# Performance work log

Measured on AMD Instinct MI355X. Metric: run time of the kernel, lower is better.

The kernel has to match this reference:

```python
import jax, jax.numpy as jnp
import numpy as np

B, N, C = 2, 8192, 256
H = 8
CH = C // H  # head dim 32
M = 32       # nbhd size
HID = 512    # mlp hidden = 2.0 * dim
TAB = 3025   # pre_table rows (55x55 relative positions)
POSF = 5     # pos_dim + 3


def _ln(x, w, b):
    mu = jnp.mean(x, axis=-1, keepdims=True)
    var = jnp.var(x, axis=-1, keepdims=True)
    return (x - mu) / jnp.sqrt(var + 1e-5) * w + b


def setup_inputs() -> dict:
    key = jax.random.key(0)
    ks = jax.random.split(key, 24)
    s = lambda fan: 1.0 / np.sqrt(fan)
    inp = {
        'feat': jax.random.normal(ks[0], (B, N, C), jnp.float32),
        'member_idx': jax.random.randint(ks[1], (B, N, M), 0, N),
        'cluster_mask': jnp.ones((B, N, M), jnp.float32),
        'pe_idx': jax.random.randint(ks[2], (B, N, M), 0, TAB),
        'global_attn': 0,
        'pre_table': jax.random.normal(ks[3], (TAB, POSF), jnp.float32),
        'norm1_w': jnp.ones((C,), jnp.float32),
        'norm1_b': jnp.zeros((C,), jnp.float32),
        'q_w': jax.random.normal(ks[4], (C, C), jnp.float32) * s(C),
        'q_b': jnp.zeros((C,), jnp.float32),
        'kv_w': jax.random.normal(ks[5], (2 * C, C), jnp.float32) * s(C),
        'kv_b': jnp.zeros((2 * C,), jnp.float32),
        'blank_k': jax.random.normal(ks[6], (C,), jnp.float32),
        'blank_v': jax.random.normal(ks[7], (C,), jnp.float32),
        'pe_w': jax.random.normal(ks[8], (H, POSF), jnp.float32) * s(POSF),
        'pe_b': jnp.zeros((H,), jnp.float32),
        'proj_w': jax.random.normal(ks[9], (C, C), jnp.float32) * s(C),
        'proj_b': jnp.zeros((C,), jnp.float32),
        'norm2_w': jnp.ones((C,), jnp.float32),
        'norm2_b': jnp.zeros((C,), jnp.float32),
        'fc1_w': jax.random.normal(ks[10], (HID, C), jnp.float32) * s(C),
        'fc1_b': jnp.zeros((HID,), jnp.float32),
        'fc2_w': jax.random.normal(ks[11], (C, HID), jnp.float32) * s(HID),
        'fc2_b': jnp.zeros((C,), jnp.float32),
    }
    return inp


def _block(feat, member_idx, cluster_mask, pe_idx, pre_table,
           norm1_w, norm1_b, q_w, q_b, kv_w, kv_b, blank_k, blank_v,
           pe_w, pe_b, proj_w, proj_b, norm2_w, norm2_b,
           fc1_w, fc1_b, fc2_w, fc2_b):
    b, n, c = feat.shape
    h, c_ = H, c // H
    scale = c_ ** -0.5
    shortcut = feat
    x = _ln(feat, norm1_w, norm1_b)
    q = (x @ q_w.T + q_b) * scale                     # b n c
    kv = (x @ kv_w.T + kv_b).reshape(b, n, h, 2, c_)  # torch view layout
    k = kv[..., 0, :]                                 # b n h c_
    v = kv[..., 1, :]
    q = q.reshape(b, n, h, c_)
    bidx = jnp.arange(b)[:, None, None]
    k_g = k[bidx, member_idx]                         # b n m h c_ (gather)
    attn = jnp.einsum('bnhc,bnmhc->bhnm', q, k_g)     # CLUSTENQK
    pe_table = pre_table @ pe_w.T + pe_b              # TAB h
    pos = pe_table[pe_idx]                            # b n m h
    attn = attn + pos.transpose(0, 3, 1, 2)
    attn = attn + (1.0 - cluster_mask)[:, None, :, :] * (-100.0)
    blank = jnp.einsum('bnhc,hc->bhn', q, blank_k.reshape(h, c_))
    blank = jnp.clip(blank, -5.0, 5.0)[..., None]     # b h n 1
    attn = jnp.concatenate([attn, blank], axis=-1)
    attn = jax.nn.softmax(attn, axis=-1)
    blank_a = attn[..., -1:]
    attn = attn[..., :-1]
    v_g = v[bidx, member_idx]                         # b n m h c_
    out = jnp.einsum('bhnm,bnmhc->bnhc', attn, v_g)   # CLUSTENAV
    out = out + blank_a.transpose(0, 2, 1, 3) * blank_v.reshape(1, 1, h, c_)
    out = out.reshape(b, n, c)
    out = out @ proj_w.T + proj_b
    x = shortcut + out
    y = _ln(x, norm2_w, norm2_b)
    y = jax.nn.gelu(y @ fc1_w.T + fc1_b, approximate=False)
    y = y @ fc2_w.T + fc2_b
    return x + y


def reference(feat, member_idx, cluster_mask, pe_idx, global_attn, pre_table,
              norm1_w, norm1_b, q_w, q_b, kv_w, kv_b, blank_k, blank_v,
              pe_w, pe_b, proj_w, proj_b, norm2_w, norm2_b,
              fc1_w, fc1_b, fc2_w, fc2_b):
    # global_attn is False (local cluster attention path)
    return _block(feat, member_idx, cluster_mask, pe_idx, pre_table,
                  norm1_w, norm1_b, q_w, q_b, kv_w, kv_b, blank_k, blank_v,
                  pe_w, pe_b, proj_w, proj_b, norm2_w, norm2_b,
                  fc1_w, fc1_b, fc2_w, fc2_b)
```

## Files before the change

### kernel.cpp

```cpp
#include <hip/hip_runtime.h>
#include <math.h>

namespace {
constexpr int kN    = 8192;
constexpr int kC    = 256;
constexpr int kRowsTotal = 2 * kN;
constexpr float kScale = 0.17677669529663687f;
}

typedef __attribute__((ext_vector_type(8))) short bf16x8;
typedef __attribute__((ext_vector_type(4))) float f32x4;
typedef _Float16 h8 __attribute__((ext_vector_type(8)));
typedef _Float16 h4 __attribute__((ext_vector_type(4)));

__device__ __forceinline__ unsigned short f2bf(float f) {
  unsigned int u = __float_as_uint(f);
  u += 0x7fffu + ((u >> 16) & 1u);
  return (unsigned short)(u >> 16);
}
__device__ __forceinline__ float bflo(unsigned int u) {
  return __uint_as_float(u << 16);
}
__device__ __forceinline__ float bfhi(unsigned int u) {
  return __uint_as_float(u & 0xffff0000u);
}
__device__ __forceinline__ unsigned short f2h(float f) {
  _Float16 h = (_Float16)f;
  unsigned short u;
  __builtin_memcpy(&u, &h, 2);
  return u;
}
__device__ __forceinline__ float h2f(unsigned short u) {
  _Float16 h;
  __builtin_memcpy(&h, &u, 2);
  return (float)h;
}

#define GLOAD16(g, l)                                                   \
  __builtin_amdgcn_global_load_lds(                                     \
      (const __attribute__((address_space(1))) void*)(g),               \
      (__attribute__((address_space(3))) void*)(l), 16, 0, 0)

__global__ __launch_bounds__(256) void prep_kernel(
    const float* __restrict__ qw, const float* __restrict__ kvw,
    const float* __restrict__ pjw, const float* __restrict__ f1w,
    const float* __restrict__ f2w, const float* __restrict__ qb,
    const float* __restrict__ kvb, const float* __restrict__ bk,
    const float* __restrict__ feat, const float* __restrict__ n1w,
    const float* __restrict__ n1b, const int* __restrict__ pe_idx,
    const float* __restrict__ pre_table, const float* __restrict__ pe_w,
    const float* __restrict__ pe_b, const float* __restrict__ cmask,
    unsigned short* __restrict__ wqkv, unsigned short* __restrict__ wproj,
    unsigned short* __restrict__ wfc1, unsigned short* __restrict__ wfc2,
    float* __restrict__ bqkv, unsigned short* __restrict__ bkh,
    unsigned short* __restrict__ xln, unsigned short* __restrict__ posm) {
  int bid = blockIdx.x;
  int t = threadIdx.x;
  if (bid < 2052) {
    int i = bid * 256 + t;
    if (i < 65536)       wqkv[i]            = f2bf(qw[i]);
    else if (i < 196608) wqkv[i]            = f2bf(kvw[i - 65536]);
    else if (i < 262144) wproj[i - 196608]  = f2bf(pjw[i - 196608]);
    else if (i < 393216) wfc1[i - 262144]   = f2bf(f1w[i - 262144]);
    else if (i < 524288) wfc2[i - 393216]   = f2bf(f2w[i - 393216]);
    else if (i < 524544) bqkv[i - 524288]   = qb[i - 524288];
    else if (i < 525056) bqkv[i - 524288]   = kvb[i - 524544];
    else if (i < 525312) bkh[i - 525056]    = f2h(bk[i - 525056]);
  } else if (bid < 6148) {
    int row = (bid - 2052) * 4 + (t >> 6);
    int l = t & 63;
    float4 v = *(const float4*)(feat + (size_t)row * kC + l * 4);
    float s  = v.x + v.y + v.z + v.w;
    float s2 = v.x * v.x + v.y * v.y + v.z * v.z + v.w * v.w;
#pragma unroll
    for (int d = 1; d < 64; d <<= 1) {
      s  += __shfl_xor(s, d, 64);
      s2 += __shfl_xor(s2, d, 64);
    }
    float mu = s * (1.0f / kC);
    float rstd = rsqrtf(s2 * (1.0f / kC) - mu * mu + 1e-5f);
    float4 wv = *(const float4*)(n1w + l * 4);
    float4 bv = *(const float4*)(n1b + l * 4);
    uint2 ov;
    ov.x = ((unsigned int)f2bf((v.y - mu) * rstd * wv.y + bv.y) << 16) |
           f2bf((v.x - mu) * rstd * wv.x + bv.x);
    ov.y = ((unsigned int)f2bf((v.w - mu) * rstd * wv.w + bv.w) << 16) |
           f2bf((v.z - mu) * rstd * wv.z + bv.z);
    *(uint2*)(xln + (size_t)row * kC + l * 4) = ov;
  } else {
    int i = (bid - 6148) * 256 + t;
    int row = i >> 8, m = (i >> 3) & 31, h = i & 7;
    int idx = pe_idx[(size_t)row * 32 + m];
    float acc = pe_b[h];
#pragma unroll
    for (int f = 0; f < 5; ++f)
      acc += pre_table[idx * 5 + f] * pe_w[h * 5 + f];
    acc += (1.0f - cmask[(size_t)row * 32 + m]) * -100.0f;
    posm[(size_t)row * 256 + h * 32 + m] = f2h(acc);
  }
}

template <int EPI, int KDIM>
__global__ __launch_bounds__(512) void gemm64(
    const unsigned short* __restrict__ A, const unsigned short* __restrict__ Wt,
    const float* __restrict__ bias, void* __restrict__ o1,
    unsigned short* __restrict__ o2, unsigned short* __restrict__ o3) {
  __shared__ alignas(16) unsigned short smem[40960];
  unsigned short* As0 = smem;
  unsigned short* Bs0 = smem + 8192;
  int t = threadIdx.x;
  int w = t >> 6, l = t & 63;
  int bm = blockIdx.x * 64, bn = blockIdx.y * 256;

  f32x4 acc[4][2] = {};

  const size_t aoff = (size_t)(bm + w * 8 + (l >> 3)) * KDIM + (l & 7) * 8;
  const size_t boff = (size_t)(bn + w * 32 + (l >> 3)) * KDIM + (l & 7) * 8;
  const int lr = l & 15, lk = l >> 4;

#define STAGE_T(buf, k0)                                                      \
  do {                                                                        \
    GLOAD16(A + aoff + (k0), As0 + (buf)*4096 + w * 512 + l * 8);             \
    GLOAD16(Wt + boff + (k0), Bs0 + (buf)*16384 + w * 2048 + l * 8);          \
    GLOAD16(Wt + boff + (k0) + (size_t)8 * KDIM,                              \
            Bs0 + (buf)*16384 + w * 2048 + 512 + l * 8);                      \
    GLOAD16(Wt + boff + (k0) + (size_t)16 * KDIM,                             \
            Bs0 + (buf)*16384 + w * 2048 + 1024 + l * 8);                     \
    GLOAD16(Wt + boff + (k0) + (size_t)24 * KDIM,                             \
            Bs0 + (buf)*16384 + w * 2048 + 1536 + l * 8);                     \
  } while (0)

  auto compute = [&](int buf) {
#pragma unroll
    for (int kk = 0; kk < 2; ++kk) {
      bf16x8 af[4], bfr[2];
#pragma unroll
      for (int mi = 0; mi < 4; ++mi)
        af[mi] = *(const bf16x8*)(As0 + buf * 4096 + (mi * 16 + lr) * 64 +
                                  kk * 32 + lk * 8);
#pragma unroll
      for (int ni = 0; ni < 2; ++ni)
        bfr[ni] = *(const bf16x8*)(Bs0 + buf * 16384 +
                                   (w * 32 + ni * 16 + lr) * 64 + kk * 32 +
                                   lk * 8);
#pragma unroll
      for (int mi = 0; mi < 4; ++mi)
#pragma unroll
        for (int ni = 0; ni < 2; ++ni)
          acc[mi][ni] = __builtin_amdgcn_mfma_f32_16x16x32_bf16(
              af[mi], bfr[ni], acc[mi][ni], 0, 0, 0);
    }
  };

  STAGE_T(0, 0);
  __syncthreads();
  int cur = 0;
#pragma unroll
  for (int k0 = 64; k0 < KDIM; k0 += 64) {
    STAGE_T(cur ^ 1, k0);
    compute(cur);
    __syncthreads();
    cur ^= 1;
  }
  compute(cur);

#pragma unroll
  for (int mi = 0; mi < 4; ++mi) {
#pragma unroll
    for (int ni = 0; ni < 2; ++ni) {
      int col = bn + w * 32 + ni * 16 + lr;
      float bv = bias[col];
#pragma unroll
      for (int j = 0; j < 4; ++j) {
        int rg = bm + mi * 16 + lk * 4 + j;
        float x = acc[mi][ni][j] + bv;
        if (col < 256) {
          ((unsigned short*)o1)[(size_t)rg * 256 + col] = f2h(x * kScale);
        } else {
          int c = col - 256;
          int h = c >> 6, sbit = (c >> 5) & 1, ch = c & 31;
          unsigned short* dst = sbit ? o3 : o2;
          dst[(size_t)rg * 256 + h * 32 + ch] = f2h(x);
        }
      }
    }
  }
#undef STAGE_T
}

__global__ __launch_bounds__(512) void mlp_fused(
    const unsigned short* __restrict__ A,
    const unsigned short* __restrict__ Wp,
    const float* __restrict__ pbias,
    const float* __restrict__ feat,
    const float* __restrict__ w2, const float* __restrict__ b2,
    const unsigned short* __restrict__ W1, const float* __restrict__ b1,
    const unsigned short* __restrict__ W2, const float* __restrict__ b2f,
    float* __restrict__ outp) {
  __shared__ alignas(16) unsigned short sm[66560];
  int t = threadIdx.x;
  int w = t >> 6, l = t & 63;
  int bm = blockIdx.x * 64;
  const int lr = l & 15, lk = l >> 4;

  f32x4 accp[4][2] = {};
  {
    const size_t aoff = (size_t)(bm + w * 8 + (l >> 3)) * 256 + (l & 7) * 8;
    const size_t boff = (size_t)(w * 32 + (l >> 3)) * 256 + (l & 7) * 8;
#define PSTAGE(buf, k0)                                                       \
  do {                                                                        \
    GLOAD16(A + aoff + (k0), sm + (buf)*4096 + w * 512 + l * 8);              \
    GLOAD16(Wp + boff + (k0), sm + 8192 + (buf)*16384 + w * 2048 + l * 8);    \
    GLOAD16(Wp + boff + (k0) + (size_t)2048,                                  \
            sm + 8192 + (buf)*16384 + w * 2048 + 512 + l * 8);                \
    GLOAD16(Wp + boff + (k0) + (size_t)4096,                                  \
            sm + 8192 + (buf)*16384 + w * 2048 + 1024 + l * 8);               \
    GLOAD16(Wp + boff + (k0) + (size_t)6144,                                  \
            sm + 8192 + (buf)*16384 + w * 2048 + 1536 + l * 8);               \
  } while (0)
    auto computeP = [&](int buf) {
#pragma unroll
      for (int kk = 0; kk < 2; ++kk) {
        bf16x8 af[4], bfr[2];
#pragma unroll
        for (int mi = 0; mi < 4; ++mi)
          af[mi] = *(const bf16x8*)(sm + buf * 4096 + (mi * 16 + lr) * 64 +
                                    kk * 32 + lk * 8);
#pragma unroll
        for (int ni = 0; ni < 2; ++ni)
          bfr[ni] = *(const bf16x8*)(sm + 8192 + buf * 16384 +
                                     (w * 32 + ni * 16 + lr) * 64 + kk * 32 +
                                     lk * 8);
#pragma unroll
        for (int mi = 0; mi < 4; ++mi)
#pragma unroll
          for (int ni = 0; ni < 2; ++ni)
            accp[mi][ni] = __builtin_amdgcn_mfma_f32_16x16x32_bf16(
                af[mi], bfr[ni], accp[mi][ni], 0, 0, 0);
      }
    };
    PSTAGE(0, 0);
    __syncthreads();
    int cur = 0;
#pragma unroll
    for (int k0 = 64; k0 < 256; k0 += 64) {
      PSTAGE(cur ^ 1, k0);
      computeP(cur);
      __syncthreads();
      cur ^= 1;
    }
    computeP(cur);
#undef PSTAGE
  }

  f32x4 xr[4][2];
  float* xs = (float*)sm;
  __syncthreads();
#pragma unroll
  for (int mi = 0; mi < 4; ++mi) {
#pragma unroll
    for (int ni = 0; ni < 2; ++ni) {
      int c = w * 32 + ni * 16 + lr;
      float bv = pbias[c];
#pragma unroll
      for (int j = 0; j < 4; ++j) {
        int rl = mi * 16 + lk * 4 + j;
        float x = accp[mi][ni][j] + bv + feat[(size_t)(bm + rl) * 256 + c];
        xr[mi][ni][j] = x;
        xs[rl * 260 + c] = x;
      }
    }
  }
  __syncthreads();

  {
    int r = t >> 3, sub = t & 7;
    float4 xv[8];
    float sx = 0.f, sxx = 0.f;
#pragma unroll
    for (int i = 0; i < 8; ++i) {
      xv[i] = *(const float4*)&xs[r * 260 + sub * 4 + i * 32];
      sx  += xv[i].x + xv[i].y + xv[i].z + xv[i].w;
      sxx += xv[i].x * xv[i].x + xv[i].y * xv[i].y + xv[i].z * xv[i].z +
             xv[i].w * xv[i].w;
    }
#pragma unroll
    for (int d = 1; d < 8; d <<= 1) {
      sx  += __shfl_xor(sx, d, 64);
      sxx += __shfl_xor(sxx, d, 64);
    }
    float mu = sx * (1.0f / 256.0f);
    float rstd = rsqrtf(sxx * (1.0f / 256.0f) - mu * mu + 1e-5f);
#pragma unroll
    for (int i = 0; i < 8; ++i) {
      int c = sub * 4 + i * 32;
      float4 wv = *(const float4*)(w2 + c);
      float4 bv = *(const float4*)(b2 + c);
      uint2 ov;
      ov.x = ((unsigned int)f2bf((xv[i].y - mu) * rstd * wv.y + bv.y) << 16) |
             f2bf((xv[i].x - mu) * rstd * wv.x + bv.x);
      ov.y = ((unsigned int)f2bf((xv[i].w - mu) * rstd * wv.w + bv.w) << 16) |
             f2bf((xv[i].z - mu) * rstd * wv.z + bv.z);
      *(uint2*)&sm[49664 + r * 264 + c] = ov;
    }
  }
  __syncthreads();

  const int FB = 33280;
#define F1STAGE(buf, k0, c)                                                   \
  do {                                                                        \
    GLOAD16(W1 + (size_t)((c)*256 + w * 32 + (l >> 2)) * 256 + (k0) +         \
                (l & 3) * 8,                                                  \
            sm + FB + (buf)*8192 + w * 1024 + l * 8);                         \
    GLOAD16(W1 + (size_t)((c)*256 + w * 32 + 16 + (l >> 2)) * 256 + (k0) +    \
                (l & 3) * 8,                                                  \
            sm + FB + (buf)*8192 + w * 1024 + 512 + l * 8);                   \
  } while (0)
#pragma unroll
  for (int c = 0; c < 2; ++c) {
    f32x4 accf[4][2] = {};
    auto computeF1 = [&](int buf, int ka) {
      bf16x8 af[4], bfr[2];
#pragma unroll
      for (int mi = 0; mi < 4; ++mi)
        af[mi] =
            *(const bf16x8*)(sm + 49664 + (mi * 16 + lr) * 264 + ka + lk * 8);
#pragma unroll
      for (int ni = 0; ni < 2; ++ni)
        bfr[ni] = *(const bf16x8*)(sm + FB + buf * 8192 +
                                   (w * 32 + ni * 16 + lr) * 32 + lk * 8);
#pragma unroll
      for (int mi = 0; mi < 4; ++mi)
#pragma unroll
        for (int ni = 0; ni < 2; ++ni)
          accf[mi][ni] = __builtin_amdgcn_mfma_f32_16x16x32_bf16(
              af[mi], bfr[ni], accf[mi][ni], 0, 0, 0);
    };
    F1STAGE(0, 0, c);
    __syncthreads();
    int cur = 0;
#pragma unroll
    for (int k0 = 32; k0 < 256; k0 += 32) {
      F1STAGE(cur ^ 1, k0, c);
      computeF1(cur, k0 - 32);
      __syncthreads();
      cur ^= 1;
    }
    computeF1(cur, 224);
    __syncthreads();
#pragma unroll
    for (int mi = 0; mi < 4; ++mi) {
#pragma unroll
      for (int ni = 0; ni < 2; ++ni) {
        int colg = c * 256 + w * 32 + ni * 16 + lr;
        float bv = b1[colg];
#pragma unroll
        for (int j = 0; j < 4; ++j) {
          float x = accf[mi][ni][j] + bv;
          float g = 0.5f * x * (1.0f + erff(x * 0.70710678118654752f));
          sm[(mi * 16 + lk * 4 + j) * 520 + colg] = f2bf(g);
        }
      }
    }
  }
#undef F1STAGE
  __syncthreads();

  f32x4 acc2[4][2] = {};
#define F2STAGE(buf, k0)                                                      \
  do {                                                                        \
    GLOAD16(W2 + (size_t)(w * 32 + (l >> 3)) * 512 + (k0) + (l & 7) * 8,      \
            sm + FB + (buf)*16384 + w * 2048 + l * 8);                        \
    GLOAD16(W2 + (size_t)(w * 32 + 8 + (l >> 3)) * 512 + (k0) + (l & 7) * 8,  \
            sm + FB + (buf)*16384 + w * 2048 + 512 + l * 8);                  \
    GLOAD16(W2 + (size_t)(w * 32 + 16 + (l >> 3)) * 512 + (k0) + (l & 7) * 8, \
            sm + FB + (buf)*16384 + w * 2048 + 1024 + l * 8);                 \
    GLOAD16(W2 + (size_t)(w * 32 + 24 + (l >> 3)) * 512 + (k0) + (l & 7) * 8, \
            sm + FB + (buf)*16384 + w * 2048 + 1536 + l * 8);                 \
  } while (0)
  {
    auto computeF2 = [&](int buf, int ka) {
#pragma unroll
      for (int kk = 0; kk < 2; ++kk) {
        bf16x8 af[4], bfr[2];
#pragma unroll
        for (int mi = 0; mi < 4; ++mi)
          af[mi] = *(const bf16x8*)(sm + (mi * 16 + lr) * 520 + ka + kk * 32 +
                                    lk * 8);
#pragma unroll
        for (int ni = 0; ni < 2; ++ni)
          bfr[ni] = *(const bf16x8*)(sm + FB + buf * 16384 +
                                     (w * 32 + ni * 16 + lr) * 64 + kk * 32 +
                                     lk * 8);
#pragma unroll
        for (int mi = 0; mi < 4; ++mi)
#pragma unroll
          for (int ni = 0; ni < 2; ++ni)
            acc2[mi][ni] = __builtin_amdgcn_mfma_f32_16x16x32_bf16(
                af[mi], bfr[ni], acc2[mi][ni], 0, 0, 0);
      }
    };
    F2STAGE(0, 0);
    __syncthreads();
    int cur = 0;
#pragma unroll
    for (int k0 = 64; k0 < 512; k0 += 64) {
      F2STAGE(cur ^ 1, k0);
      computeF2(cur, k0 - 64);
      __syncthreads();
      cur ^= 1;
    }
    computeF2(cur, 448);
  }
#undef F2STAGE

#pragma unroll
  for (int mi = 0; mi < 4; ++mi) {
#pragma unroll
    for (int ni = 0; ni < 2; ++ni) {
      int col = w * 32 + ni * 16 + lr;
      float bv = b2f[col];
#pragma unroll
      for (int j = 0; j < 4; ++j) {
        int rg = bm + mi * 16 + lk * 4 + j;
        outp[(size_t)rg * 256 + col] = xr[mi][ni][j] + acc2[mi][ni][j] + bv;
      }
    }
  }
}

__global__ __launch_bounds__(256) void attn_kernel(
    const unsigned short* __restrict__ q, const unsigned short* __restrict__ k,
    const unsigned short* __restrict__ v, const int* __restrict__ member_idx,
    const unsigned short* __restrict__ posm,
    const unsigned short* __restrict__ bkh, const float* __restrict__ blank_v,
    unsigned short* __restrict__ outp) {
  int t = threadIdx.x;
  int w = t >> 6, l = t & 63;
  int bid = blockIdx.x;
  int part = bid & 7;
  int bb = part >> 2, hg = part & 3;
  int row = bb * kN + (bid >> 3) * 4 + w;
  const unsigned int kvbyte = (unsigned int)bb * (kN * 512u);

  __shared__ float        aw[4][2][36];
  __shared__ unsigned int offs[4][32];
  __shared__ float        posl[4][2][32];

  {
    int m = l & 31, hloc = l >> 5;
    posl[w][hloc][m] = h2f(posm[(size_t)row * 256 + hg * 64 + l]);
    if (l < 32)
      offs[w][l] =
          kvbyte + (unsigned int)member_idx[(size_t)row * 32 + l] * 512u;
  }
  __syncthreads();

  const int m8 = l >> 3, ch = l & 7;
  const int hsel = ch >> 2;

  h8 qv8 = *(const h8*)(q + (size_t)row * 256 + hg * 64 + ch * 8);

  float lg[4];
#pragma unroll
  for (int i = 0; i < 4; ++i) {
    int mi = i * 8 + m8;
    const char* kp = (const char*)k + offs[w][mi] + hg * 128 + ch * 16;
    h8 kv = *(const h8*)kp;
    float p = 0.f;
#pragma unroll
    for (int e = 0; e < 8; ++e) p = fmaf((float)qv8[e], (float)kv[e], p);
    p += __shfl_xor(p, 1, 64);
    p += __shfl_xor(p, 2, 64);
    lg[i] = p + posl[w][hsel][mi];
  }

  float bl = 0.f;
  {
    h8 bk8 = *(const h8*)(bkh + hg * 64 + ch * 8);
#pragma unroll
    for (int e = 0; e < 8; ++e) bl = fmaf((float)qv8[e], (float)bk8[e], bl);
    bl += __shfl_xor(bl, 1, 64);
    bl += __shfl_xor(bl, 2, 64);
    bl = fminf(fmaxf(bl, -5.0f), 5.0f);
  }

  float mx = fmaxf(fmaxf(lg[0], lg[1]), fmaxf(lg[2], lg[3]));
  mx = fmaxf(mx, __shfl_xor(mx, 8, 64));
  mx = fmaxf(mx, __shfl_xor(mx, 16, 64));
  mx = fmaxf(mx, __shfl_xor(mx, 32, 64));
  mx = fmaxf(mx, bl);
  float e4[4], s = 0.f;
#pragma unroll
  for (int i = 0; i < 4; ++i) { e4[i] = __expf(lg[i] - mx); s += e4[i]; }
  s += __shfl_xor(s, 8, 64);
  s += __shfl_xor(s, 16, 64);
  s += __shfl_xor(s, 32, 64);
  float eb = __expf(bl - mx);
  s += eb;
  float inv = __builtin_amdgcn_rcpf(s);
  if ((ch & 3) == 0) {
#pragma unroll
    for (int i = 0; i < 4; ++i) aw[w][hsel][i * 8 + m8] = e4[i] * inv;
    if (m8 == 0) aw[w][hsel][32] = eb * inv;
  }
  __syncthreads();

  const int hp = l >> 5, sq = (l >> 3) & 3, c8 = l & 7;
  const char* vb = (const char*)v + (hg * 2 + hp) * 64 + c8 * 8;
  float a0 = 0.f, a1 = 0.f, a2 = 0.f, a3 = 0.f;
#pragma unroll
  for (int i = 0; i < 8; ++i) {
    int mm = sq * 8 + i;
    float a = aw[w][hp][mm];
    h4 u = *(const h4*)(vb + offs[w][mm]);
    a0 = fmaf(a, (float)u[0], a0);
    a1 = fmaf(a, (float)u[1], a1);
    a2 = fmaf(a, (float)u[2], a2);
    a3 = fmaf(a, (float)u[3], a3);
  }
  a0 += __shfl_xor(a0, 8, 64);  a1 += __shfl_xor(a1, 8, 64);
  a2 += __shfl_xor(a2, 8, 64);  a3 += __shfl_xor(a3, 8, 64);
  a0 += __shfl_xor(a0, 16, 64); a1 += __shfl_xor(a1, 16, 64);
  a2 += __shfl_xor(a2, 16, 64); a3 += __shfl_xor(a3, 16, 64);
  if (sq == 0) {
    float ab = aw[w][hp][32];
    int c = (hg * 2 + hp) * 32 + c8 * 4;
    float4 bv = *(const float4*)(blank_v + c);
    a0 = fmaf(ab, bv.x, a0);
    a1 = fmaf(ab, bv.y, a1);
    a2 = fmaf(ab, bv.z, a2);
    a3 = fmaf(ab, bv.w, a3);
    uint2 o;
    o.x = ((unsigned int)f2bf(a1) << 16) | f2bf(a0);
    o.y = ((unsigned int)f2bf(a3) << 16) | f2bf(a2);
    *(uint2*)(outp + (size_t)row * 256 + c) = o;
  }
}

extern "C" void kernel_launch(void* const* d_in, const int* in_sizes, int n_in,
                              void* d_out, int out_size, void* d_ws, size_t ws_size,
                              hipStream_t stream) {
  const float* feat       = (const float*)d_in[0];
  const int*   member_idx = (const int*)d_in[1];
  const float* cmask      = (const float*)d_in[2];
  const int*   pe_idx     = (const int*)d_in[3];
  const float* pre_table  = (const float*)d_in[5];
  const float* n1w        = (const float*)d_in[6];
  const float* n1b        = (const float*)d_in[7];
  const float* q_w        = (const float*)d_in[8];
  const float* q_b        = (const float*)d_in[9];
  const float* kv_w       = (const float*)d_in[10];
  const float* kv_b       = (const float*)d_in[11];
  const float* blank_k    = (const float*)d_in[12];
  const float* blank_v    = (const float*)d_in[13];
  const float* pe_w       = (const float*)d_in[14];
  const float* pe_b       = (const float*)d_in[15];
  const float* proj_w     = (const float*)d_in[16];
  const float* proj_b     = (const float*)d_in[17];
  const float* n2w        = (const float*)d_in[18];
  const float* n2b        = (const float*)d_in[19];
  const float* fc1_w      = (const float*)d_in[20];
  const float* fc1_b      = (const float*)d_in[21];
  const float* fc2_w      = (const float*)d_in[22];
  const float* fc2_b      = (const float*)d_in[23];

  float* out = (float*)d_out;
  unsigned char* ws = (unsigned char*)d_ws;

  unsigned short* xln   = (unsigned short*)(ws + 0);
  unsigned short* q_buf = (unsigned short*)(ws + 8388608);
  unsigned short* k_buf = (unsigned short*)(ws + 16777216);
  unsigned short* v_buf = (unsigned short*)(ws + 25165824);
  unsigned short* wqkv  = (unsigned short*)(ws + 33554432);
  unsigned short* wproj = (unsigned short*)(ws + 33947648);
  unsigned short* wfc1  = (unsigned short*)(ws + 34078720);
  unsigned short* wfc2  = (unsigned short*)(ws + 34340864);
  float*          bqkv  = (float*)(ws + 34603008);
  unsigned short* bkh   = (unsigned short*)(ws + 34606080);
  unsigned short* attn_out = xln;
  unsigned short* posm  = (unsigned short*)out;

  prep_kernel<<<22532, 256, 0, stream>>>(
      q_w, kv_w, proj_w, fc1_w, fc2_w, q_b, kv_b, blank_k, feat, n1w, n1b,
      pe_idx, pre_table, pe_w, pe_b, cmask, wqkv, wproj, wfc1, wfc2, bqkv,
      bkh, xln, posm);

  gemm64<0, 256><<<dim3(kRowsTotal / 64, 3), 512, 0, stream>>>(
      xln, wqkv, bqkv, q_buf, k_buf, v_buf);

  attn_kernel<<<kRowsTotal, 256, 0, stream>>>(
      q_buf, k_buf, v_buf, member_idx, posm, bkh, blank_v, attn_out);

  mlp_fused<<<kRowsTotal / 64, 512, 0, stream>>>(
      attn_out, wproj, proj_b, feat, n2w, n2b, wfc1, fc1_b, wfc2, fc2_b, out);
}
```

Baseline: 108.7 us.

## Fuse LayerNorm1 into QKV GEMM and use fdot2 in attention logits

Removes the LayerNorm section from the prep kernel and computes LN1 inside a new qkv_fused kernel, which keeps the normalized 64-row A tile resident in shared memory and loops over the three output column blocks, streaming only weight tiles. This drops the bf16 xln round trip through global memory and one grid dimension, but each block now does three times the GEMM work serially, leaving fewer blocks (256) for the GPU. The attention kernel also replaces scalar f16-to-f32 FMAs with packed fdot2 instructions for the q·k and q·blank_k dot products.

```diff
diff --git a/kernel.cpp b/kernel.cpp
--- a/kernel.cpp
+++ b/kernel.cpp
@@ -12,17 +12,12 @@
 typedef __attribute__((ext_vector_type(4))) float f32x4;
 typedef _Float16 h8 __attribute__((ext_vector_type(8)));
 typedef _Float16 h4 __attribute__((ext_vector_type(4)));
+typedef _Float16 h2 __attribute__((ext_vector_type(2)));
 
 __device__ __forceinline__ unsigned short f2bf(float f) {
   unsigned int u = __float_as_uint(f);
   u += 0x7fffu + ((u >> 16) & 1u);
   return (unsigned short)(u >> 16);
-}
-__device__ __forceinline__ float bflo(unsigned int u) {
-  return __uint_as_float(u << 16);
-}
-__device__ __forceinline__ float bfhi(unsigned int u) {
-  return __uint_as_float(u & 0xffff0000u);
 }
 __device__ __forceinline__ unsigned short f2h(float f) {
   _Float16 h = (_Float16)f;
@@ -36,6 +31,16 @@
   return (float)h;
 }
 
+#if __has_builtin(__builtin_amdgcn_fdot2)
+__device__ __forceinline__ float fdot2f(h2 a, h2 b, float c) {
+  return __builtin_amdgcn_fdot2(a, b, c, false);
+}
+#else
+__device__ __forceinline__ float fdot2f(h2 a, h2 b, float c) {
+  return fmaf((float)a[0], (float)b[0], fmaf((float)a[1], (float)b[1], c));
+}
+#endif
+
 #define GLOAD16(g, l)                                                   \
   __builtin_amdgcn_global_load_lds(                                     \
       (const __attribute__((address_space(1))) void*)(g),               \
@@ -46,14 +51,12 @@
     const float* __restrict__ pjw, const float* __restrict__ f1w,
     const float* __restrict__ f2w, const float* __restrict__ qb,
     const float* __restrict__ kvb, const float* __restrict__ bk,
-    const float* __restrict__ feat, const float* __restrict__ n1w,
-    const float* __restrict__ n1b, const int* __restrict__ pe_idx,
-    const float* __restrict__ pre_table, const float* __restrict__ pe_w,
-    const float* __restrict__ pe_b, const float* __restrict__ cmask,
-    unsigned short* __restrict__ wqkv, unsigned short* __restrict__ wproj,
-    unsigned short* __restrict__ wfc1, unsigned short* __restrict__ wfc2,
-    float* __restrict__ bqkv, unsigned short* __restrict__ bkh,
-    unsigned short* __restrict__ xln, unsigned short* __restrict__ posm) {
+    const int* __restrict__ pe_idx, const float* __restrict__ pre_table,
+    const float* __restrict__ pe_w, const float* __restrict__ pe_b,
+    const float* __restrict__ cmask, unsigned short* __restrict__ wqkv,
+    unsigned short* __restrict__ wproj, unsigned short* __restrict__ wfc1,
+    unsigned short* __restrict__ wfc2, float* __restrict__ bqkv,
+    unsigned short* __restrict__ bkh, unsigned short* __restrict__ posm) {
   int bid = blockIdx.x;
   int t = threadIdx.x;
   if (bid < 2052) {
@@ -66,29 +69,8 @@
     else if (i < 524544) bqkv[i - 524288]   = qb[i - 524288];
     else if (i < 525056) bqkv[i - 524288]   = kvb[i - 524544];
     else if (i < 525312) bkh[i - 525056]    = f2h(bk[i - 525056]);
-  } else if (bid < 6148) {
-    int row = (bid - 2052) * 4 + (t >> 6);
-    int l = t & 63;
-    float4 v = *(const float4*)(feat + (size_t)row * kC + l * 4);
-    float s  = v.x + v.y + v.z + v.w;
-    float s2 = v.x * v.x + v.y * v.y + v.z * v.z + v.w * v.w;
-#pragma unroll
-    for (int d = 1; d < 64; d <<= 1) {
-      s  += __shfl_xor(s, d, 64);
-      s2 += __shfl_xor(s2, d, 64);
-    }
-    float mu = s * (1.0f / kC);
-    float rstd = rsqrtf(s2 * (1.0f / kC) - mu * mu + 1e-5f);
-    float4 wv = *(const float4*)(n1w + l * 4);
-    float4 bv = *(const float4*)(n1b + l * 4);
-    uint2 ov;
-    ov.x = ((unsigned int)f2bf((v.y - mu) * rstd * wv.y + bv.y) << 16) |
-           f2bf((v.x - mu) * rstd * wv.x + bv.x);
-    ov.y = ((unsigned int)f2bf((v.w - mu) * rstd * wv.w + bv.w) << 16) |
-           f2bf((v.z - mu) * rstd * wv.z + bv.z);
-    *(uint2*)(xln + (size_t)row * kC + l * 4) = ov;
   } else {
-    int i = (bid - 6148) * 256 + t;
+    int i = (bid - 2052) * 256 + t;
     int row = i >> 8, m = (i >> 3) & 31, h = i & 7;
     int idx = pe_idx[(size_t)row * 32 + m];
     float acc = pe_b[h];
@@ -100,99 +82,120 @@
   }
 }
 
-template <int EPI, int KDIM>
-__global__ __launch_bounds__(512) void gemm64(
-    const unsigned short* __restrict__ A, const unsigned short* __restrict__ Wt,
-    const float* __restrict__ bias, void* __restrict__ o1,
-    unsigned short* __restrict__ o2, unsigned short* __restrict__ o3) {
-  __shared__ alignas(16) unsigned short smem[40960];
-  unsigned short* As0 = smem;
-  unsigned short* Bs0 = smem + 8192;
+__global__ __launch_bounds__(512) void qkv_fused(
+    const float* __restrict__ feat, const float* __restrict__ n1w,
+    const float* __restrict__ n1b, const unsigned short* __restrict__ Wq,
+    const float* __restrict__ bqkv, unsigned short* __restrict__ qo,
+    unsigned short* __restrict__ ko, unsigned short* __restrict__ vo) {
+  __shared__ alignas(16) unsigned short sm[33280];
   int t = threadIdx.x;
   int w = t >> 6, l = t & 63;
-  int bm = blockIdx.x * 64, bn = blockIdx.y * 256;
-
-  f32x4 acc[4][2] = {};
-
-  const size_t aoff = (size_t)(bm + w * 8 + (l >> 3)) * KDIM + (l & 7) * 8;
-  const size_t boff = (size_t)(bn + w * 32 + (l >> 3)) * KDIM + (l & 7) * 8;
+  int bm = blockIdx.x * 64;
   const int lr = l & 15, lk = l >> 4;
-
-#define STAGE_T(buf, k0)                                                      \
+  const int BsB = 16896;
+
+  {
+    int r = t >> 3, sub = t & 7;
+    float4 xv[8];
+    float sx = 0.f, sxx = 0.f;
+#pragma unroll
+    for (int i = 0; i < 8; ++i) {
+      xv[i] = *(const float4*)(feat + (size_t)(bm + r) * 256 + sub * 4 + i * 32);
+      sx  += xv[i].x + xv[i].y + xv[i].z + xv[i].w;
+      sxx += xv[i].x * xv[i].x + xv[i].y * xv[i].y + xv[i].z * xv[i].z +
+             xv[i].w * xv[i].w;
+    }
+#pragma unroll
+    for (int d = 1; d < 8; d <<= 1) {
+      sx  += __shfl_xor(sx, d, 64);
+      sxx += __shfl_xor(sxx, d, 64);
+    }
+    float mu = sx * (1.0f / 256.0f);
+    float rstd = rsqrtf(sxx * (1.0f / 256.0f) - mu * mu + 1e-5f);
+#pragma unroll
+    for (int i = 0; i < 8; ++i) {
+      int c = sub * 4 + i * 32;
+      float4 wv = *(const float4*)(n1w + c);
+      float4 bv = *(const float4*)(n1b + c);
+      uint2 ov;
+      ov.x = ((unsigned int)f2bf((xv[i].y - mu) * rstd * wv.y + bv.y) << 16) |
+             f2bf((xv[i].x - mu) * rstd * wv.x + bv.x);
+      ov.y = ((unsigned int)f2bf((xv[i].w - mu) * rstd * wv.w + bv.w) << 16) |
+             f2bf((xv[i].z - mu) * rstd * wv.z + bv.z);
+      *(uint2*)&sm[r * 264 + c] = ov;
+    }
+  }
+
+#define QSTAGE(buf, k0, bn)                                                   \
   do {                                                                        \
-    GLOAD16(A + aoff + (k0), As0 + (buf)*4096 + w * 512 + l * 8);             \
-    GLOAD16(Wt + boff + (k0), Bs0 + (buf)*16384 + w * 2048 + l * 8);          \
-    GLOAD16(Wt + boff + (k0) + (size_t)8 * KDIM,                              \
-            Bs0 + (buf)*16384 + w * 2048 + 512 + l * 8);                      \
-    GLOAD16(Wt + boff + (k0) + (size_t)16 * KDIM,                             \
-            Bs0 + (buf)*16384 + w * 2048 + 1024 + l * 8);                     \
-    GLOAD16(Wt + boff + (k0) + (size_t)24 * KDIM,                             \
-            Bs0 + (buf)*16384 + w * 2048 + 1536 + l * 8);                     \
+    GLOAD16(Wq + (size_t)((bn)*256 + w * 32 + (l >> 2)) * 256 + (k0) +        \
+                (l & 3) * 8,                                                  \
+            sm + BsB + (buf)*8192 + w * 1024 + l * 8);                        \
+    GLOAD16(Wq + (size_t)((bn)*256 + w * 32 + 16 + (l >> 2)) * 256 + (k0) +   \
+                (l & 3) * 8,                                                  \
+            sm + BsB + (buf)*8192 + w * 1024 + 512 + l * 8);                  \
   } while (0)
 
-  auto compute = [&](int buf) {
-#pragma unroll
-    for (int kk = 0; kk < 2; ++kk) {
+#pragma unroll
+  for (int bn = 0; bn < 3; ++bn) {
+    f32x4 acc[4][2] = {};
+    auto computeQ = [&](int buf, int ka) {
       bf16x8 af[4], bfr[2];
 #pragma unroll
       for (int mi = 0; mi < 4; ++mi)
-        af[mi] = *(const bf16x8*)(As0 + buf * 4096 + (mi * 16 + lr) * 64 +
-                                  kk * 32 + lk * 8);
+        af[mi] = *(const bf16x8*)(sm + (mi * 16 + lr) * 264 + ka + lk * 8);
 #pragma unroll
       for (int ni = 0; ni < 2; ++ni)
-        bfr[ni] = *(const bf16x8*)(Bs0 + buf * 16384 +
-                                   (w * 32 + ni * 16 + lr) * 64 + kk * 32 +
-                                   lk * 8);
+        bfr[ni] = *(const bf16x8*)(sm + BsB + buf * 8192 + w * 1024 +
+                                   (ni * 16 + lr) * 32 + lk * 8);
 #pragma unroll
       for (int mi = 0; mi < 4; ++mi)
 #pragma unroll
         for (int ni = 0; ni < 2; ++ni)
           acc[mi][ni] = __builtin_amdgcn_mfma_f32_16x16x32_bf16(
               af[mi], bfr[ni], acc[mi][ni], 0, 0, 0);
-    }
-  };
-
-  STAGE_T(0, 0);
-  __syncthreads();
-  int cur = 0;
-#pragma unroll
-  for (int k0 = 64; k0 < KDIM; k0 += 64) {
-    STAGE_T(cur ^ 1, k0);
-    compute(cur);
+    };
+    QSTAGE(0, 0, bn);
     __syncthreads();
-    cur ^= 1;
-  }
-  compute(cur);
-
-#pragma unroll
-  for (int mi = 0; mi < 4; ++mi) {
-#pragma unroll
-    for (int ni = 0; ni < 2; ++ni) {
-      int col = bn + w * 32 + ni * 16 + lr;
-      float bv = bias[col];
-#pragma unroll
-      for (int j = 0; j < 4; ++j) {
-        int rg = bm + mi * 16 + lk * 4 + j;
-        float x = acc[mi][ni][j] + bv;
-        if (col < 256) {
-          ((unsigned short*)o1)[(size_t)rg * 256 + col] = f2h(x * kScale);
-        } else {
-          int c = col - 256;
-          int h = c >> 6, sbit = (c >> 5) & 1, ch = c & 31;
-          unsigned short* dst = sbit ? o3 : o2;
-          dst[(size_t)rg * 256 + h * 32 + ch] = f2h(x);
+    int cur = 0;
+#pragma unroll
+    for (int k0 = 32; k0 < 256; k0 += 32) {
+      QSTAGE(cur ^ 1, k0, bn);
+      computeQ(cur, k0 - 32);
+      __syncthreads();
+      cur ^= 1;
+    }
+    computeQ(cur, 224);
+
+#pragma unroll
+    for (int mi = 0; mi < 4; ++mi) {
+#pragma unroll
+      for (int ni = 0; ni < 2; ++ni) {
+        int col = bn * 256 + w * 32 + ni * 16 + lr;
+        float bv = bqkv[col];
+#pragma unroll
+        for (int j = 0; j < 4; ++j) {
+          int rg = bm + mi * 16 + lk * 4 + j;
+          float x = acc[mi][ni][j] + bv;
+          if (col < 256) {
+            qo[(size_t)rg * 256 + col] = f2h(x * kScale);
+          } else {
+            int c = col - 256;
+            int h = c >> 6, sbit = (c >> 5) & 1, ch = c & 31;
+            unsigned short* dst = sbit ? vo : ko;
+            dst[(size_t)rg * 256 + h * 32 + ch] = f2h(x);
+          }
         }
       }
     }
-  }
-#undef STAGE_T
+    __syncthreads();
+  }
+#undef QSTAGE
 }
 
 __global__ __launch_bounds__(512) void mlp_fused(
-    const unsigned short* __restrict__ A,
-    const unsigned short* __restrict__ Wp,
-    const float* __restrict__ pbias,
-    const float* __restrict__ feat,
+    const unsigned short* __restrict__ A, const unsigned short* __restrict__ Wp,
+    const float* __restrict__ pbias, const float* __restrict__ feat,
     const float* __restrict__ w2, const float* __restrict__ b2,
     const unsigned short* __restrict__ W1, const float* __restrict__ b1,
     const unsigned short* __restrict__ W2, const float* __restrict__ b2f,
@@ -460,6 +463,7 @@
   const int hsel = ch >> 2;
 
   h8 qv8 = *(const h8*)(q + (size_t)row * 256 + hg * 64 + ch * 8);
+  const h2* qa = (const h2*)&qv8;
 
   float lg[4];
 #pragma unroll
@@ -467,9 +471,10 @@
     int mi = i * 8 + m8;
     const char* kp = (const char*)k + offs[w][mi] + hg * 128 + ch * 16;
     h8 kv = *(const h8*)kp;
+    const h2* ka = (const h2*)&kv;
     float p = 0.f;
 #pragma unroll
-    for (int e = 0; e < 8; ++e) p = fmaf((float)qv8[e], (float)kv[e], p);
+    for (int e = 0; e < 4; ++e) p = fdot2f(qa[e], ka[e], p);
     p += __shfl_xor(p, 1, 64);
     p += __shfl_xor(p, 2, 64);
     lg[i] = p + posl[w][hsel][mi];
@@ -478,8 +483,9 @@
   float bl = 0.f;
   {
     h8 bk8 = *(const h8*)(bkh + hg * 64 + ch * 8);
-#pragma unroll
-    for (int e = 0; e < 8; ++e) bl = fmaf((float)qv8[e], (float)bk8[e], bl);
+    const h2* ba = (const h2*)&bk8;
+#pragma unroll
+    for (int e = 0; e < 4; ++e) bl = fdot2f(qa[e], ba[e], bl);
     bl += __shfl_xor(bl, 1, 64);
     bl += __shfl_xor(bl, 2, 64);
     bl = fminf(fmaxf(bl, -5.0f), 5.0f);
@@ -568,7 +574,7 @@
   float* out = (float*)d_out;
   unsigned char* ws = (unsigned char*)d_ws;
 
-  unsigned short* xln   = (unsigned short*)(ws + 0);
+  unsigned short* attn_out = (unsigned short*)(ws + 0);
   unsigned short* q_buf = (unsigned short*)(ws + 8388608);
   unsigned short* k_buf = (unsigned short*)(ws + 16777216);
   unsigned short* v_buf = (unsigned short*)(ws + 25165824);
@@ -578,16 +584,14 @@
   unsigned short* wfc2  = (unsigned short*)(ws + 34340864);
   float*          bqkv  = (float*)(ws + 34603008);
   unsigned short* bkh   = (unsigned short*)(ws + 34606080);
-  unsigned short* attn_out = xln;
   unsigned short* posm  = (unsigned short*)out;
 
-  prep_kernel<<<22532, 256, 0, stream>>>(
-      q_w, kv_w, proj_w, fc1_w, fc2_w, q_b, kv_b, blank_k, feat, n1w, n1b,
-      pe_idx, pre_table, pe_w, pe_b, cmask, wqkv, wproj, wfc1, wfc2, bqkv,
-      bkh, xln, posm);
-
-  gemm64<0, 256><<<dim3(kRowsTotal / 64, 3), 512, 0, stream>>>(
-      xln, wqkv, bqkv, q_buf, k_buf, v_buf);
+  prep_kernel<<<18436, 256, 0, stream>>>(
+      q_w, kv_w, proj_w, fc1_w, fc2_w, q_b, kv_b, blank_k, pe_idx, pre_table,
+      pe_w, pe_b, cmask, wqkv, wproj, wfc1, wfc2, bqkv, bkh, posm);
+
+  qkv_fused<<<kRowsTotal / 64, 512, 0, stream>>>(
+      feat, n1w, n1b, wqkv, bqkv, q_buf, k_buf, v_buf);
 
   attn_kernel<<<kRowsTotal, 256, 0, stream>>>(
       q_buf, k_buf, v_buf, member_idx, posm, bkh, blank_v, attn_out);
```

New measurement: 110.7 us. No clear change (+1.8%).
